# Kernel optimization log

Hardware: AMD Instinct MI355X
Metric: run time of the kernel (lower is better)

Reference implementation:

```python
import jax, jax.numpy as jnp
import numpy as np

D = 256; H = 4; HD = 64; WBAND = 64; KLOC = 8; EMAK = 256
SUMDECAY = 0.9; STATEDECAY = 0.9; STEP = 0.5


def _dwconv(x, kern, pad):
    # x: (B,T,D), kern: (D,1,K) cross-correlation taps, causal left pad
    lhs = jnp.transpose(x, (0, 2, 1))
    out = jax.lax.conv_general_dilated(
        lhs, kern, (1,), [(pad, 0)],
        dimension_numbers=('NCH', 'OIH', 'NCH'),
        feature_group_count=x.shape[-1])
    return jnp.transpose(out, (0, 2, 1))


def _ln(x, g, b):
    m = jnp.mean(x, -1, keepdims=True)
    v = jnp.var(x, -1, keepdims=True)
    return (x - m) * jax.lax.rsqrt(v + 1e-5) * g + b


def _lin(x, w, b):
    return jnp.dot(x, w.T) + b


def _forward(parallel_repr, sequential_state, trajectory_summary, conv_w, conv_b,
             qkv_w, qkv_b, mo_w, mo_b, fg_w, fg_b, gkv_w, gkv_b, go_w, go_b,
             comb_w, comb_b, ffn1_w, ffn1_b, ffn2_w, ffn2_b, tr1_w, tr1_b,
             tr2_w, tr2_b, p2s_w, p2s_b, s2p_w, s2p_b,
             ln1_g, ln1_b, ln2_g, ln2_b, ln3_g, ln3_b, ln4_g, ln4_b):
    B, T, _ = parallel_repr.shape
    # Tier 1: local depthwise causal conv (window 8); torch pads both sides then slices [:T] == causal left pad
    local_history = _dwconv(parallel_repr, conv_w, KLOC - 1) + conv_b
    # Tier 2: banded causal attention (keep j in [i-63, i])
    qkv = _lin(parallel_repr, qkv_w, qkv_b).reshape(B, T, 3, H, HD)
    qkv = jnp.transpose(qkv, (2, 0, 3, 1, 4))  # (3,B,H,T,HD)
    q, k, v = qkv[0], qkv[1], qkv[2]
    idx = jnp.arange(T)
    band = (idx[:, None] >= idx[None, :]) & (idx[None, :] > idx[:, None] - WBAND)
    scores = jnp.einsum('bhqd,bhkd->bhqk', q, k) / jnp.sqrt(jnp.float32(HD))
    attn = jax.nn.softmax(jnp.where(band, scores, -1e9), -1)
    med = jnp.einsum('bhqk,bhkd->bhqd', attn, v)
    med = jnp.transpose(med, (0, 2, 1, 3)).reshape(B, T, D)
    med = _lin(med, mo_w, mo_b)
    fg = jax.nn.sigmoid(_lin(jnp.concatenate([parallel_repr, med], -1), fg_w, fg_b))
    medium_out = med * fg
    # Tier 3: causal cumulative (linear-attention style) global concepts
    gkv = _lin(parallel_repr, gkv_w, gkv_b)
    gk, gv = jnp.split(gkv, 2, -1)
    gk = jax.nn.elu(gk) + 1.0
    concepts = jnp.cumsum(gk * gv, 1) / (jnp.cumsum(gk, 1) + 1e-5)
    global_out = _lin(concepts, go_w, go_b)
    combined = _lin(jnp.concatenate([local_history, medium_out, global_out], -1), comb_w, comb_b)
    pr = _ln(parallel_repr + combined, ln1_g, ln1_b)
    # EMA summary via 256-tap causal depthwise conv: w[i] = (1-d)*d^i
    kE = min(T, EMAK)
    taps = (1.0 - SUMDECAY) * SUMDECAY ** jnp.arange(kE, dtype=jnp.float32)
    kern = jnp.broadcast_to(taps[::-1][None, None, :], (D, 1, kE))
    global_summary = _dwconv(pr, kern, kE - 1)
    guidance = _lin(pr, p2s_w, p2s_b)
    cs = jnp.concatenate([pr + 0.3 * guidance, global_summary], -1)
    deltas = jnp.tanh(_lin(jax.nn.gelu(_lin(cs, tr1_w, tr1_b), approximate=False), tr2_w, tr2_b))
    scaled = deltas * STEP
    # state accumulation via conv trick: acc[t] = sum_i d^i * delta[t-i]
    staps = STATEDECAY ** jnp.arange(kE, dtype=jnp.float32)
    skern = jnp.broadcast_to(staps[::-1][None, None, :], (D, 1, kE))
    acc = _dwconv(scaled, skern, kE - 1)
    dpow = STATEDECAY ** jnp.arange(1, T + 1, dtype=jnp.float32)
    pre_ln = sequential_state[:, None, :] * dpow[None, :, None] + acc
    states = _ln(pre_ln, ln3_g, ln3_b)
    seq_g = _lin(states, s2p_w, s2p_b)
    ffn = _lin(jax.nn.gelu(_lin(pr + 0.3 * seq_g, ffn1_w, ffn1_b), approximate=False), ffn2_w, ffn2_b)
    pr_out = _ln(pr + ffn, ln2_g, ln2_b)
    final_state = _ln(states[:, -1, :], ln4_g, ln4_b)
    final_traj = global_summary[:, -1, :]
    return pr_out, final_state, final_traj


def setup_inputs():
    key = jax.random.key(0)
    ks = jax.random.split(key, 20)
    B, T = 4, 2048
    s = 0.02
    def w(i, shape):
        return jax.random.normal(ks[i], shape, jnp.float32) * s
    return {
        'parallel_repr': jax.random.normal(ks[0], (B, T, D), jnp.float32),
        'sequential_state': jax.random.normal(ks[1], (B, D), jnp.float32),
        'trajectory_summary': jax.random.normal(ks[2], (B, D), jnp.float32),
        'conv_w': w(3, (D, 1, KLOC)), 'conv_b': jnp.zeros((D,)),
        'qkv_w': w(4, (3 * D, D)), 'qkv_b': jnp.zeros((3 * D,)),
        'mo_w': w(5, (D, D)), 'mo_b': jnp.zeros((D,)),
        'fg_w': w(6, (D, 2 * D)), 'fg_b': jnp.zeros((D,)),
        'gkv_w': w(7, (2 * D, D)), 'gkv_b': jnp.zeros((2 * D,)),
        'go_w': w(8, (D, D)), 'go_b': jnp.zeros((D,)),
        'comb_w': w(9, (D, 3 * D)), 'comb_b': jnp.zeros((D,)),
        'ffn1_w': w(10, (4 * D, D)), 'ffn1_b': jnp.zeros((4 * D,)),
        'ffn2_w': w(11, (D, 4 * D)), 'ffn2_b': jnp.zeros((D,)),
        'tr1_w': w(12, (2 * D, 2 * D)), 'tr1_b': jnp.zeros((2 * D,)),
        'tr2_w': w(13, (D, 2 * D)), 'tr2_b': jnp.zeros((D,)),
        'p2s_w': w(14, (D, D)), 'p2s_b': jnp.zeros((D,)),
        's2p_w': w(15, (D, D)), 's2p_b': jnp.zeros((D,)),
        'ln1_g': jnp.ones((D,)), 'ln1_b': jnp.zeros((D,)),
        'ln2_g': jnp.ones((D,)), 'ln2_b': jnp.zeros((D,)),
        'ln3_g': jnp.ones((D,)), 'ln3_b': jnp.zeros((D,)),
        'ln4_g': jnp.ones((D,)), 'ln4_b': jnp.zeros((D,)),
    }


def reference(parallel_repr, sequential_state, trajectory_summary, conv_w, conv_b,
              qkv_w, qkv_b, mo_w, mo_b, fg_w, fg_b, gkv_w, gkv_b, go_w, go_b,
              comb_w, comb_b, ffn1_w, ffn1_b, ffn2_w, ffn2_b, tr1_w, tr1_b,
              tr2_w, tr2_b, p2s_w, p2s_b, s2p_w, s2p_b,
              ln1_g, ln1_b, ln2_g, ln2_b, ln3_g, ln3_b, ln4_g, ln4_b):
    return _forward(parallel_repr, sequential_state, trajectory_summary, conv_w, conv_b,
                    qkv_w, qkv_b, mo_w, mo_b, fg_w, fg_b, gkv_w, gkv_b, go_w, go_b,
                    comb_w, comb_b, ffn1_w, ffn1_b, ffn2_w, ffn2_b, tr1_w, tr1_b,
                    tr2_w, tr2_b, p2s_w, p2s_b, s2p_w, s2p_b,
                    ln1_g, ln1_b, ln2_g, ln2_b, ln3_g, ln3_b, ln4_g, ln4_b)
```

## Files before the change

kernel.cpp:

```cpp
#include <hip/hip_runtime.h>
#include <hip/hip_bf16.h>
#include <math.h>

#define D_  256
#define T_  2048
#define B_  4
#define M_  (B_*T_)
#define H_  4
#define HD_ 64

#define NC_ 64
#define LCH (T_/NC_)

enum { OP_NONE=0, OP_SIGMUL=1, OP_ADDAUX=2, OP_AXPBY=3, OP_GELU=4, OP_TANHHALF=5 };

typedef unsigned short u16;
typedef short short8 __attribute__((ext_vector_type(8)));
typedef float f32x4  __attribute__((ext_vector_type(4)));

__device__ __forceinline__ float gelu_f(float x){ return 0.5f*x*(1.0f+erff(x*0.70710678118654752f)); }
__device__ __forceinline__ float sigmoid_f(float x){ return 1.0f/(1.0f+expf(-x)); }

__device__ __forceinline__ unsigned pk2(float a, float b){
    __hip_bfloat162 h = __float22bfloat162_rn(make_float2(a,b));
    union { __hip_bfloat162 h; unsigned u; } c; c.h = h; return c.u;
}
__device__ __forceinline__ float bfu(u16 u){ return __uint_as_float(((unsigned)u)<<16); }
__device__ __forceinline__ u16 bf1(float x){ return (u16)(pk2(x,x)&0xffffu); }

#define OFF_QKV   0u
#define OFF_MO    327680u
#define OFF_FG    393216u
#define OFF_GO    524288u
#define OFF_COMB  589824u
#define OFF_FFN1  786432u
#define OFF_FFN2  1048576u
#define OFF_TR1   1310720u
#define OFF_TR2   1572864u
#define OFF_P2S   1703936u
#define OFF_S2P   1769472u
#define NWELEM    1835008u
#define NXELEM    2097152u
#define CVT_BLKS  3842u
#define CONV_BLKS 2048u

__global__ __launch_bounds__(256) void cvt_conv_k(
    const float* __restrict__ qkv_w, const float* __restrict__ gkv_w,
    const float* __restrict__ qkv_b, const float* __restrict__ gkv_b,
    const float* __restrict__ mo_w,  const float* __restrict__ fg_w,
    const float* __restrict__ go_w,  const float* __restrict__ comb_w,
    const float* __restrict__ ffn1_w,const float* __restrict__ ffn2_w,
    const float* __restrict__ tr1_w, const float* __restrict__ tr2_w,
    const float* __restrict__ p2s_w, const float* __restrict__ s2p_w,
    const float* __restrict__ X,
    const float* __restrict__ conv_w, const float* __restrict__ conv_b,
    u16* __restrict__ Wh, u16* __restrict__ Xh, float* __restrict__ bq,
    u16* __restrict__ LH)
{
    if (blockIdx.x >= CVT_BLKS){
        int idx = (blockIdx.x - CVT_BLKS)*256 + threadIdx.x;
        int d4 = (idx & 63) * 4;
        int bt = idx >> 6;
        int t = bt & (T_-1);
        float a0 = conv_b[d4], a1 = conv_b[d4+1], a2 = conv_b[d4+2], a3 = conv_b[d4+3];
        const float* xp = X + (size_t)bt*D_ + d4;
        #pragma unroll
        for (int j=0;j<8;++j){
            int tt = t - 7 + j;
            if (tt >= 0){
                float4 v = *(const float4*)(xp + (size_t)(j-7)*D_);
                a0 += v.x * conv_w[(d4+0)*8 + j];
                a1 += v.y * conv_w[(d4+1)*8 + j];
                a2 += v.z * conv_w[(d4+2)*8 + j];
                a3 += v.w * conv_w[(d4+3)*8 + j];
            }
        }
        *(uint2*)(LH + (size_t)bt*D_ + d4) = (uint2){ pk2(a0,a1), pk2(a2,a3) };
        return;
    }
    size_t i = ((size_t)blockIdx.x*256 + threadIdx.x)*4;
    if (i < NWELEM){
        const float* s; size_t base;
        if      (i < OFF_MO)  { s=(i<196608)?qkv_w:gkv_w; base=(i<196608)?0:196608; }
        else if (i < OFF_FG)  { s=mo_w;   base=OFF_MO; }
        else if (i < OFF_GO)  { s=fg_w;   base=OFF_FG; }
        else if (i < OFF_COMB){ s=go_w;   base=OFF_GO; }
        else if (i < OFF_FFN1){ s=comb_w; base=OFF_COMB; }
        else if (i < OFF_FFN2){ s=ffn1_w; base=OFF_FFN1; }
        else if (i < OFF_TR1) { s=ffn2_w; base=OFF_FFN2; }
        else if (i < OFF_TR2) { s=tr1_w;  base=OFF_TR1; }
        else if (i < OFF_P2S) { s=tr2_w;  base=OFF_TR2; }
        else if (i < OFF_S2P) { s=p2s_w;  base=OFF_P2S; }
        else                  { s=s2p_w;  base=OFF_S2P; }
        float4 v = *(const float4*)(s + (i-base));
        *(uint2*)(Wh + i) = (uint2){ pk2(v.x,v.y), pk2(v.z,v.w) };
    } else if (i < NWELEM + NXELEM){
        size_t j = i - NWELEM;
        float4 v = *(const float4*)(X + j);
        *(uint2*)(Xh + j) = (uint2){ pk2(v.x,v.y), pk2(v.z,v.w) };
    } else if (i < NWELEM + NXELEM + 1280){
        size_t j = i - (NWELEM + NXELEM);
        #pragma unroll
        for (int k=0;k<4;++k){
            size_t e = j + k;
            bq[e] = (e < 768) ? qkv_b[e] : gkv_b[e-768];
        }
    }
}

__global__ __launch_bounds__(512) void gemm_k(
    const u16* __restrict__ A0, const u16* __restrict__ W0, int ldw0, int K0,
    const u16* __restrict__ A1, const u16* __restrict__ W1, int ldw1, int K1,
    const u16* __restrict__ A2, const u16* __restrict__ W2, int ldw2, int K2,
    const float* __restrict__ bias, const void* __restrict__ aux, int aux_bf16,
    void* __restrict__ C, int ldc, int c_bf16, int op, int ncol)
{
    __shared__ u16 As[128*64];
    __shared__ u16 Ws[64*64];

    const int q8   = gridDim.x >> 3;
    const int lid  = (blockIdx.x & 7)*q8 + (blockIdx.x >> 3);
    const int brow = lid / ncol;
    const int bcol = lid - brow*ncol;
    const int row0 = brow*128, col0 = bcol*64;

    const int tid  = threadIdx.x;
    const int lane = tid & 63, wid = tid >> 6;
    const int wm = (wid >> 1)*32, wn = (wid & 1)*32;
    const int l15 = lane & 15, l4 = lane >> 4;
    const int rowA = tid >> 2;
    const int scA  = (tid & 3) * 8;
    const int rowW = tid >> 3;
    const int scW  = (tid & 7) * 8;

    f32x4 acc[2][2];
    #pragma unroll
    for (int i=0;i<2;++i)
        #pragma unroll
        for (int j=0;j<2;++j) acc[i][j] = (f32x4){0.f,0.f,0.f,0.f};

    uint4 ra0, ra1, rw0;

    auto loadtile = [&](const u16* A, const u16* W, int ldw, int K, int kb){
        const u16* ga = A + (size_t)(row0+rowA)*K + kb + scA;
        ra0 = *(const uint4*)ga;
        ra1 = *(const uint4*)(ga + 32);
        rw0 = *(const uint4*)(W + (size_t)(col0+rowW)*ldw + kb + scW);
    };
    auto storetile = [&](){
        const int sw = (rowA&7)<<3;
        *(uint4*)&As[(rowA*64 + scA) ^ sw]      = ra0;
        *(uint4*)&As[(rowA*64 + scA + 32) ^ sw] = ra1;
        *(uint4*)&Ws[(rowW*64 + scW) ^ ((rowW&7)<<3)] = rw0;
    };
    auto mfma_tile = [&](){
        #pragma unroll
        for (int ks=0;ks<2;++ks){
            const int koff = ks*32 + l4*8;
            short8 af[2], bf[2];
            #pragma unroll
            for (int f=0;f<2;++f){
                const int ar = wm + f*16 + l15;
                af[f] = *(const short8*)&As[(ar*64 + koff) ^ ((ar&7)<<3)];
                const int brn = wn + f*16 + l15;
                bf[f] = *(const short8*)&Ws[(brn*64 + koff) ^ ((brn&7)<<3)];
            }
            #pragma unroll
            for (int fm=0;fm<2;++fm)
                #pragma unroll
                for (int fn=0;fn<2;++fn)
                    acc[fm][fn] = __builtin_amdgcn_mfma_f32_16x16x32_bf16(
                        af[fm], bf[fn], acc[fm][fn], 0, 0, 0);
        }
    };

    const u16* Ac = A0; const u16* Wc = W0; int ldwc = ldw0, Kc = K0, kb = 0;
    loadtile(Ac, Wc, ldwc, Kc, 0);
    while (true){
        __syncthreads();
        storetile();
        __syncthreads();
        int nkb = kb + 64;
        const u16* nA = Ac; const u16* nW = Wc; int nld = ldwc, nK = Kc;
        bool have_next = true;
        if (nkb >= Kc){
            if (Ac == A0 && A1){ nA = A1; nW = W1; nld = ldw1; nK = K1; nkb = 0; }
            else if (Ac == A1 && A2){ nA = A2; nW = W2; nld = ldw2; nK = K2; nkb = 0; }
            else have_next = false;
        }
        if (have_next) loadtile(nA, nW, nld, nK, nkb);
        mfma_tile();
        if (!have_next) break;
        Ac = nA; Wc = nW; ldwc = nld; Kc = nK; kb = nkb;
    }

    #pragma unroll
    for (int fn=0;fn<2;++fn){
        const int n = col0 + wn + fn*16 + l15;
        const float bv = bias[n];
        #pragma unroll
        for (int fm=0;fm<2;++fm){
            #pragma unroll
            for (int j=0;j<4;++j){
                const int m = row0 + wm + fm*16 + l4*4 + j;
                float v = acc[fm][fn][j] + bv;
                if (op==OP_GELU)          v = gelu_f(v);
                else if (op==OP_TANHHALF) v = 0.5f*tanhf(v);
                else if (op!=OP_NONE){
                    const size_t ai = (size_t)m*D_ + n;
                    const float a = aux_bf16 ? bfu(((const u16*)aux)[ai])
                                             : ((const float*)aux)[ai];
                    if (op==OP_SIGMUL)      v = a*sigmoid_f(v);
                    else if (op==OP_ADDAUX) v = v + a;
                    else                    v = a + 0.3f*v;
                }
                if (c_bf16) ((u16*)C)[(size_t)m*ldc + n] = bf1(v);
                else        ((float*)C)[(size_t)m*ldc + n] = v;
            }
        }
    }
}

__global__ __launch_bounds__(256) void attn_k(const u16* __restrict__ QKVG,
    u16* __restrict__ MED)
{
    __shared__ u16 Kl[128*64];
    __shared__ u16 Ql[64*64];
    __shared__ u16 Vl[64*128];
    const int b = blockIdx.z, h = blockIdx.y;
    const int t0 = blockIdx.x * 64;
    const int kb0 = t0 - 64;
    const int tid = threadIdx.x;

    {
        const int r0 = tid >> 3, c8 = (tid & 7) * 8;
        #pragma unroll
        for (int rep=0;rep<4;++rep){
            const int r = r0 + rep*32;
            const int kg = kb0 + r;
            uint4 pk = {0,0,0,0}, pv = {0,0,0,0};
            if (kg >= 0){
                const u16* gp = QKVG + ((size_t)(b*T_ + kg))*1280 + h*HD_ + c8;
                pk = *(const uint4*)(gp + 256);
                pv = *(const uint4*)(gp + 512);
            }
            *(uint4*)&Kl[(r*64 + c8) ^ ((r&7)<<3)] = pk;
            const u16* pvu = (const u16*)&pv;
            #pragma unroll
            for (int j=0;j<8;++j){
                const int d = c8 + j;
                Vl[(d*128 + r) ^ ((d&15)<<3)] = pvu[j];
            }
        }
        #pragma unroll
        for (int rep=0;rep<2;++rep){
            const int r = r0 + rep*32;
            uint4 pq = *(const uint4*)(QKVG + ((size_t)(b*T_ + t0 + r))*1280 + h*HD_ + c8);
            *(uint4*)&Ql[(r*64 + c8) ^ ((r&7)<<3)] = pq;
        }
    }
    __syncthreads();

    const int lane = tid & 63, w = tid >> 6;
    const int l15 = lane & 15, l4 = lane >> 4;

    short8 bq[2];
    {
        const int qr = w*16 + l15;
        bq[0] = *(const short8*)&Ql[(qr*64 +      l4*8) ^ ((qr&7)<<3)];
        bq[1] = *(const short8*)&Ql[(qr*64 + 32 + l4*8) ^ ((qr&7)<<3)];
    }

    f32x4 s[8];
    #pragma unroll
    for (int kf=0;kf<8;++kf){
        const int kr = kf*16 + l15;
        short8 a0 = *(const short8*)&Kl[(kr*64 +      l4*8) ^ ((kr&7)<<3)];
        short8 a1 = *(const short8*)&Kl[(kr*64 + 32 + l4*8) ^ ((kr&7)<<3)];
        f32x4 acc = (f32x4){0.f,0.f,0.f,0.f};
        acc = __builtin_amdgcn_mfma_f32_16x16x32_bf16(a0, bq[0], acc, 0,0,0);
        acc = __builtin_amdgcn_mfma_f32_16x16x32_bf16(a1, bq[1], acc, 0,0,0);
        s[kf] = acc;
    }

    const int qg = t0 + w*16 + l15;
    float m = -1e30f;
    #pragma unroll
    for (int kf=0;kf<8;++kf){
        #pragma unroll
        for (int j=0;j<4;++j){
            const int kg = kb0 + kf*16 + l4*4 + j;
            const int diff = qg - kg;
            const float v = (kg >= 0 && diff >= 0 && diff < 64) ? s[kf][j]*0.125f : -1e30f;
            s[kf][j] = v;
            m = fmaxf(m, v);
        }
    }
    m = fmaxf(m, __shfl_xor(m,16));
    m = fmaxf(m, __shfl_xor(m,32));
    float lsum = 0.f;
    unsigned lo[8], hi[8];
    #pragma unroll
    for (int kf=0;kf<8;++kf){
        const float p0 = expf(s[kf][0]-m), p1 = expf(s[kf][1]-m);
        const float p2 = expf(s[kf][2]-m), p3 = expf(s[kf][3]-m);
        lsum += (p0+p1)+(p2+p3);
        lo[kf] = pk2(p0,p1);
        hi[kf] = pk2(p2,p3);
    }
    lsum += __shfl_xor(lsum,16);
    lsum += __shfl_xor(lsum,32);
    const float inv = 1.f/lsum;

    f32x4 o[4];
    #pragma unroll
    for (int df=0;df<4;++df) o[df] = (f32x4){0.f,0.f,0.f,0.f};
    const int baseLane = l15 + ((l4&1)<<5);
    const bool hiHalf = (l4>>1) != 0;
    #pragma unroll
    for (int kb=0;kb<4;++kb){
        const int x0 = __shfl((int)lo[2*kb],   baseLane);
        const int x1 = __shfl((int)hi[2*kb],   baseLane);
        const int x2 = __shfl((int)lo[2*kb],   baseLane+16);
        const int x3 = __shfl((int)hi[2*kb],   baseLane+16);
        const int y0 = __shfl((int)lo[2*kb+1], baseLane);
        const int y1 = __shfl((int)hi[2*kb+1], baseLane);
        const int y2 = __shfl((int)lo[2*kb+1], baseLane+16);
        const int y3 = __shfl((int)hi[2*kb+1], baseLane+16);
        int4 afi;
        afi.x = hiHalf ? y0 : x0;
        afi.y = hiHalf ? y1 : x1;
        afi.z = hiHalf ? y2 : x2;
        afi.w = hiHalf ? y3 : x3;
        union { int4 i; short8 s; } cv; cv.i = afi;
        #pragma unroll
        for (int df=0;df<4;++df){
            const int vr = df*16 + l15;
            short8 bv = *(const short8*)&Vl[(vr*128 + kb*32 + l4*8) ^ ((vr&15)<<3)];
            o[df] = __builtin_amdgcn_mfma_f32_16x16x32_bf16(cv.s, bv, o[df], 0,0,0);
        }
    }

    #pragma unroll
    for (int j=0;j<4;++j){
        const float invj = __shfl(inv, l4*4 + j);
        const int mrow = b*T_ + t0 + w*16 + l4*4 + j;
        u16* op = MED + (size_t)mrow*D_ + h*HD_ + l15;
        #pragma unroll
        for (int df=0;df<4;++df)
            op[df*16] = bf1(o[df][j] * invj);
    }
}

__global__ __launch_bounds__(256) void scan1_p1(const u16* __restrict__ QKVG,
    float* __restrict__ CA, float* __restrict__ CC)
{
    const int d = threadIdx.x, c = blockIdx.x, b = blockIdx.y;
    const u16* base = QKVG + ((size_t)(b*T_ + c*LCH))*1280;
    float sgk=0.f, sgkv=0.f;
    for (int t=0;t<LCH;++t){
        float gk = bfu(base[(size_t)t*1280 + 768 + d]);
        gk = gk > 0.f ? gk + 1.f : expf(gk);
        float gv = bfu(base[(size_t)t*1280 + 1024 + d]);
        sgk += gk; sgkv += gk*gv;
    }
    CA[((size_t)b*NC_ + c)*D_ + d] = sgk;
    CC[((size_t)b*NC_ + c)*D_ + d] = sgkv;
}

__global__ __launch_bounds__(256) void scan1_p3(const u16* __restrict__ QKVG,
    const float* __restrict__ CA, const float* __restrict__ CC, u16* __restrict__ CONC)
{
    const int d = threadIdx.x, c = blockIdx.x, b = blockIdx.y;
    float sgk = 0.f, sgkv = 0.f;
    for (int cc=0; cc<c; ++cc){
        sgk  += CA[((size_t)b*NC_ + cc)*D_ + d];
        sgkv += CC[((size_t)b*NC_ + cc)*D_ + d];
    }
    const u16* base = QKVG + ((size_t)(b*T_ + c*LCH))*1280;
    u16* out = CONC + ((size_t)(b*T_ + c*LCH))*D_ + d;
    for (int t=0;t<LCH;++t){
        float gk = bfu(base[(size_t)t*1280 + 768 + d]);
        gk = gk > 0.f ? gk + 1.f : expf(gk);
        float gv = bfu(base[(size_t)t*1280 + 1024 + d]);
        sgk += gk; sgkv += gk*gv;
        out[(size_t)t*D_] = bf1(sgkv / (sgk + 1e-5f));
    }
}

__global__ __launch_bounds__(256) void ema_p1h(const u16* __restrict__ X,
    float* __restrict__ CARRY, float alpha)
{
    const int d = threadIdx.x, c = blockIdx.x, b = blockIdx.y;
    const u16* xp = X + ((size_t)(b*T_ + c*LCH))*D_ + d;
    float g = 0.f;
    for (int t=0;t<LCH;++t) g = 0.9f*g + alpha*bfu(xp[(size_t)t*D_]);
    CARRY[((size_t)b*NC_ + c)*D_ + d] = g;
}

__global__ __launch_bounds__(256) void ema_p3h(const u16* __restrict__ X,
    const float* __restrict__ CARRY, u16* __restrict__ OUT, float alpha,
    float* __restrict__ traj)
{
    const int d = threadIdx.x, c = blockIdx.x, b = blockIdx.y;
    const float dL = powf(0.9f, (float)LCH);
    float g = 0.f;
    for (int cc=0; cc<c; ++cc) g = CARRY[((size_t)b*NC_ + cc)*D_ + d] + dL*g;
    const u16* xp = X + ((size_t)(b*T_ + c*LCH))*D_ + d;
    u16* op = OUT + ((size_t)(b*T_ + c*LCH))*D_ + d;
    for (int t=0;t<LCH;++t){
        g = 0.9f*g + alpha*bfu(xp[(size_t)t*D_]);
        op[(size_t)t*D_] = bf1(g);
    }
    if (c == NC_-1) traj[b*D_ + d] = g;
}

__global__ __launch_bounds__(256) void ln1ema_k(const u16* __restrict__ in,
    const float* __restrict__ g, const float* __restrict__ b,
    u16* __restrict__ out, float* __restrict__ CARRY)
{
    __shared__ float wacc[4][256];
    const int c = blockIdx.x, bb = blockIdx.y;
    const int w = threadIdx.x >> 6, lane = threadIdx.x & 63;
    const int db = lane*4;
    const int row0 = bb*T_ + c*LCH;
    float acc0=0.f, acc1=0.f, acc2=0.f, acc3=0.f;
    #pragma unroll
    for (int it=0; it<8; ++it){
        const int r = it*4 + w;
        uint2 u = *(const uint2*)(in + (size_t)(row0 + r)*D_ + db);
        float x0=bfu((u16)(u.x&0xffff)), x1=bfu((u16)(u.x>>16));
        float x2=bfu((u16)(u.y&0xffff)), x3=bfu((u16)(u.y>>16));
        float s  = x0+x1+x2+x3;
        float s2 = x0*x0+x1*x1+x2*x2+x3*x3;
        #pragma unroll
        for (int o=1;o<64;o<<=1){ s += __shfl_xor(s,o); s2 += __shfl_xor(s2,o); }
        float mean = s*(1.f/256.f);
        float var  = s2*(1.f/256.f) - mean*mean;
        float rs = rsqrtf(var + 1e-5f);
        float y0=(x0-mean)*rs*g[db+0]+b[db+0];
        float y1=(x1-mean)*rs*g[db+1]+b[db+1];
        float y2=(x2-mean)*rs*g[db+2]+b[db+2];
        float y3=(x3-mean)*rs*g[db+3]+b[db+3];
        *(uint2*)(out + (size_t)(row0+r)*D_ + db) = (uint2){ pk2(y0,y1), pk2(y2,y3) };
        const float wt = 0.1f*powf(0.9f, (float)(31-r));
        acc0 += wt*y0; acc1 += wt*y1; acc2 += wt*y2; acc3 += wt*y3;
    }
    wacc[w][db+0]=acc0; wacc[w][db+1]=acc1; wacc[w][db+2]=acc2; wacc[w][db+3]=acc3;
    __syncthreads();
    const int d = threadIdx.x;
    CARRY[((size_t)bb*NC_ + c)*D_ + d] =
        wacc[0][d] + wacc[1][d] + wacc[2][d] + wacc[3][d];
}

__global__ __launch_bounds__(256) void ema_ln3_k(const u16* __restrict__ X,
    const float* __restrict__ CARRY, const float* __restrict__ SEQ,
    const float* __restrict__ g3, const float* __restrict__ b3, u16* __restrict__ states,
    const float* __restrict__ g4, const float* __restrict__ b4, float* __restrict__ fsout)
{
    __shared__ float vals[LCH][256];
    __shared__ float mv[LCH][2];
    __shared__ float st4[256];
    __shared__ float red[8];
    const int d = threadIdx.x, c = blockIdx.x, bb = blockIdx.y;
    const float dL = powf(0.9f, (float)LCH);
    float a = 0.f;
    for (int cc=0; cc<c; ++cc) a = CARRY[((size_t)bb*NC_ + cc)*D_ + d] + dL*a;
    const float ss = SEQ[bb*D_ + d];
    float dp = powf(0.9f, (float)(c*LCH + 1));
    const u16* xp = X + ((size_t)(bb*T_ + c*LCH))*D_ + d;
    for (int t=0;t<LCH;++t){
        a = 0.9f*a + bfu(xp[(size_t)t*D_]);
        vals[t][d] = fmaf(ss, dp, a);
        dp *= 0.9f;
    }
    __syncthreads();
    {
        const int r = threadIdx.x >> 3, seg = threadIdx.x & 7;
        float s=0.f, s2=0.f;
        #pragma unroll
        for (int j=0;j<32;++j){ float v = vals[r][seg*32+j]; s += v; s2 += v*v; }
        s += __shfl_xor(s,1); s2 += __shfl_xor(s2,1);
        s += __shfl_xor(s,2); s2 += __shfl_xor(s2,2);
        s += __shfl_xor(s,4); s2 += __shfl_xor(s2,4);
        if (seg == 0){
            float mean = s*(1.f/256.f);
            float var  = s2*(1.f/256.f) - mean*mean;
            mv[r][0] = mean; mv[r][1] = rsqrtf(var + 1e-5f);
        }
    }
    __syncthreads();
    const float gd = g3[d], bd = b3[d];
    const bool isLast = (c == NC_-1);
    u16* sp = states + ((size_t)(bb*T_ + c*LCH))*D_ + d;
    for (int t=0;t<LCH;++t){
        float st = (vals[t][d] - mv[t][0])*mv[t][1]*gd + bd;
        sp[(size_t)t*D_] = bf1(st);
        if (isLast && t == LCH-1) st4[d] = st;
    }
    if (isLast){
        __syncthreads();
        float v = st4[d];
        float s = v, s2 = v*v;
        #pragma unroll
        for (int o=1;o<64;o<<=1){ s += __shfl_xor(s,o); s2 += __shfl_xor(s2,o); }
        if ((threadIdx.x & 63) == 0){ red[threadIdx.x>>6] = s; red[4+(threadIdx.x>>6)] = s2; }
        __syncthreads();
        float S  = red[0]+red[1]+red[2]+red[3];
        float S2 = red[4]+red[5]+red[6]+red[7];
        float m2 = S*(1.f/256.f);
        float r2 = rsqrtf(S2*(1.f/256.f) - m2*m2 + 1e-5f);
        fsout[bb*D_ + d] = (st4[d]-m2)*r2*g4[d] + b4[d];
    }
}

__global__ __launch_bounds__(256) void ln2h_k(const u16* __restrict__ in,
    const float* __restrict__ g, const float* __restrict__ b, float* __restrict__ out)
{
    int row  = blockIdx.x*4 + (threadIdx.x>>6);
    int lane = threadIdx.x & 63;
    uint2 u = *(const uint2*)(in + (size_t)row*D_ + lane*4);
    float x0=bfu((u16)(u.x&0xffff)), x1=bfu((u16)(u.x>>16));
    float x2=bfu((u16)(u.y&0xffff)), x3=bfu((u16)(u.y>>16));
    float s  = x0+x1+x2+x3;
    float s2 = x0*x0+x1*x1+x2*x2+x3*x3;
    #pragma unroll
    for (int o=1;o<64;o<<=1){ s += __shfl_xor(s,o); s2 += __shfl_xor(s2,o); }
    float mean = s * (1.f/256.f);
    float var  = s2 * (1.f/256.f) - mean*mean;
    float rs = rsqrtf(var + 1e-5f);
    int db = lane*4;
    float4 r;
    r.x=(x0-mean)*rs*g[db+0]+b[db+0];
    r.y=(x1-mean)*rs*g[db+1]+b[db+1];
    r.z=(x2-mean)*rs*g[db+2]+b[db+2];
    r.w=(x3-mean)*rs*g[db+3]+b[db+3];
    *(float4*)(out + (size_t)row*D_ + db) = r;
}

extern "C" void kernel_launch(void* const* d_in, const int* in_sizes, int n_in,
                              void* d_out, int out_size, void* d_ws, size_t ws_size,
                              hipStream_t stream)
{
    const float* X     = (const float*)d_in[0];
    const float* SEQ   = (const float*)d_in[1];
    const float* conv_w= (const float*)d_in[3];
    const float* conv_b= (const float*)d_in[4];
    const float* qkv_w = (const float*)d_in[5];
    const float* qkv_b = (const float*)d_in[6];
    const float* mo_w  = (const float*)d_in[7];
    const float* mo_b  = (const float*)d_in[8];
    const float* fg_w  = (const float*)d_in[9];
    const float* fg_b  = (const float*)d_in[10];
    const float* gkv_w = (const float*)d_in[11];
    const float* gkv_b = (const float*)d_in[12];
    const float* go_w  = (const float*)d_in[13];
    const float* go_b  = (const float*)d_in[14];
    const float* comb_w= (const float*)d_in[15];
    const float* comb_b= (const float*)d_in[16];
    const float* ffn1_w= (const float*)d_in[17];
    const float* ffn1_b= (const float*)d_in[18];
    const float* ffn2_w= (const float*)d_in[19];
    const float* ffn2_b= (const float*)d_in[20];
    const float* tr1_w = (const float*)d_in[21];
    const float* tr1_b = (const float*)d_in[22];
    const float* tr2_w = (const float*)d_in[23];
    const float* tr2_b = (const float*)d_in[24];
    const float* p2s_w = (const float*)d_in[25];
    const float* p2s_b = (const float*)d_in[26];
    const float* s2p_w = (const float*)d_in[27];
    const float* s2p_b = (const float*)d_in[28];
    const float* ln1_g = (const float*)d_in[29];
    const float* ln1_b = (const float*)d_in[30];
    const float* ln2_g = (const float*)d_in[31];
    const float* ln2_b = (const float*)d_in[32];
    const float* ln3_g = (const float*)d_in[33];
    const float* ln3_b = (const float*)d_in[34];
    const float* ln4_g = (const float*)d_in[35];
    const float* ln4_b = (const float*)d_in[36];

    char* p = (char*)d_ws;
    auto alloc = [&](size_t bytes)->char*{ char* r = p; p += (bytes + 255) & ~(size_t)255; return r; };

    u16*   QKVG = (u16*)  alloc((size_t)M_*1280*2);
    u16*   Wh   = (u16*)  alloc((size_t)NWELEM*2);
    float* bq   = (float*)alloc(1280*4);
    u16*   Xh   = (u16*)  alloc((size_t)M_*256*2);
    u16*   MED  = (u16*)  alloc((size_t)M_*256*2);
    u16*   MED2 = (u16*)  alloc((size_t)M_*256*2);
    u16*   LH   = (u16*)  alloc((size_t)M_*256*2);
    u16*   CONC = (u16*)  alloc((size_t)M_*256*2);
    u16*   GOUT = (u16*)  alloc((size_t)M_*256*2);
    u16*   MOUT = (u16*)  alloc((size_t)M_*256*2);
    u16*   PRE1h= (u16*)  alloc((size_t)M_*256*2);
    u16*   PRh  = (u16*)  alloc((size_t)M_*256*2);
    u16*   GSUM = (u16*)  alloc((size_t)M_*256*2);
    u16*   CS1  = (u16*)  alloc((size_t)M_*256*2);
    u16*   H1   = (u16*)  alloc((size_t)M_*512*2);
    u16*   SCALEDh=(u16*) alloc((size_t)M_*256*2);
    u16*   STATESh=(u16*) alloc((size_t)M_*256*2);
    u16*   FFNIN= (u16*)  alloc((size_t)M_*256*2);
    u16*   H2   = (u16*)  alloc((size_t)M_*1024*2);
    u16*   PRE2h= (u16*)  alloc((size_t)M_*256*2);
    float* CAR0 = (float*)alloc((size_t)B_*NC_*D_*4);
    float* CAR1 = (float*)alloc((size_t)B_*NC_*D_*4);

    float* out_pr = (float*)d_out;
    float* out_fs = out_pr + (size_t)M_*256;
    float* out_tj = out_fs + B_*256;

    const dim3 blk256(256), blk512(512);
    const dim3 scan_grid(NC_, B_);
    const int NRg = M_/128;

    cvt_conv_k<<<dim3(CVT_BLKS + CONV_BLKS), blk256, 0, stream>>>(
        qkv_w, gkv_w, qkv_b, gkv_b, mo_w, fg_w, go_w, comb_w,
        ffn1_w, ffn2_w, tr1_w, tr2_w, p2s_w, s2p_w, X, conv_w, conv_b,
        Wh, Xh, bq, LH);
    gemm_k<<<dim3(NRg*20), blk512, 0, stream>>>(
        Xh, Wh+OFF_QKV, 256, 256,  nullptr,nullptr,0,0,  nullptr,nullptr,0,0,
        bq, nullptr, 0, QKVG, 1280, 1, OP_NONE, 20);
    attn_k<<<dim3(T_/64, H_, B_), blk256, 0, stream>>>(QKVG, MED);
    gemm_k<<<dim3(NRg*4), blk512, 0, stream>>>(
        MED, Wh+OFF_MO, 256, 256,  nullptr,nullptr,0,0,  nullptr,nullptr,0,0,
        mo_b, nullptr, 0, MED2, 256, 1, OP_NONE, 4);
    scan1_p1<<<scan_grid, blk256, 0, stream>>>(QKVG, CAR0, CAR1);
    scan1_p3<<<scan_grid, blk256, 0, stream>>>(QKVG, CAR0, CAR1, CONC);
    gemm_k<<<dim3(NRg*4), blk512, 0, stream>>>(
        CONC, Wh+OFF_GO, 256, 256,  nullptr,nullptr,0,0,  nullptr,nullptr,0,0,
        go_b, nullptr, 0, GOUT, 256, 1, OP_NONE, 4);
    gemm_k<<<dim3(NRg*4), blk512, 0, stream>>>(
        Xh, Wh+OFF_FG, 512, 256,  MED2, Wh+OFF_FG+256, 512, 256,  nullptr,nullptr,0,0,
        fg_b, MED2, 1, MOUT, 256, 1, OP_SIGMUL, 4);
    gemm_k<<<dim3(NRg*4), blk512, 0, stream>>>(
        LH, Wh+OFF_COMB, 768, 256,  MOUT, Wh+OFF_COMB+256, 768, 256,  GOUT, Wh+OFF_COMB+512, 768, 256,
        comb_b, X, 0, PRE1h, 256, 1, OP_ADDAUX, 4);
    ln1ema_k<<<scan_grid, blk256, 0, stream>>>(PRE1h, ln1_g, ln1_b, PRh, CAR0);
    ema_p3h<<<scan_grid, blk256, 0, stream>>>(PRh, CAR0, GSUM, 0.1f, out_tj);
    gemm_k<<<dim3(NRg*4), blk512, 0, stream>>>(
        PRh, Wh+OFF_P2S, 256, 256,  nullptr,nullptr,0,0,  nullptr,nullptr,0,0,
        p2s_b, PRh, 1, CS1, 256, 1, OP_AXPBY, 4);
    gemm_k<<<dim3(NRg*8), blk512, 0, stream>>>(
        CS1, Wh+OFF_TR1, 512, 256,  GSUM, Wh+OFF_TR1+256, 512, 256,  nullptr,nullptr,0,0,
        tr1_b, nullptr, 0, H1, 512, 1, OP_GELU, 8);
    gemm_k<<<dim3(NRg*4), blk512, 0, stream>>>(
        H1, Wh+OFF_TR2, 512, 512,  nullptr,nullptr,0,0,  nullptr,nullptr,0,0,
        tr2_b, nullptr, 0, SCALEDh, 256, 1, OP_TANHHALF, 4);
    ema_p1h<<<scan_grid, blk256, 0, stream>>>(SCALEDh, CAR0, 1.0f);
    ema_ln3_k<<<scan_grid, blk256, 0, stream>>>(
        SCALEDh, CAR0, SEQ, ln3_g, ln3_b, STATESh, ln4_g, ln4_b, out_fs);
    gemm_k<<<dim3(NRg*4), blk512, 0, stream>>>(
        STATESh, Wh+OFF_S2P, 256, 256,  nullptr,nullptr,0,0,  nullptr,nullptr,0,0,
        s2p_b, PRh, 1, FFNIN, 256, 1, OP_AXPBY, 4);
    gemm_k<<<dim3(NRg*16), blk512, 0, stream>>>(
        FFNIN, Wh+OFF_FFN1, 256, 256,  nullptr,nullptr,0,0,  nullptr,nullptr,0,0,
        ffn1_b, nullptr, 0, H2, 1024, 1, OP_GELU, 16);
    gemm_k<<<dim3(NRg*4), blk512, 0, stream>>>(
        H2, Wh+OFF_FFN2, 1024, 1024,  nullptr,nullptr,0,0,  nullptr,nullptr,0,0,
        ffn2_b, PRh, 1, PRE2h, 256, 1, OP_ADDAUX, 4);
    ln2h_k<<<dim3(M_/4), blk256, 0, stream>>>(PRE2h, ln2_g, ln2_b, out_pr);
}
```

Before: 253.4 us.

## Co-schedule scan and EMA phases as extra blocks inside attention and GEMM launches

Folds the scan pass-1 into the attention kernel as extra blocks, the scan pass-3 into the MO-projection GEMM launch, and the EMA pass-3 into the P2S GEMM launch, using a block-index split. This removes three separate launches and lets the latency-bound serial scans run alongside independent GEMM/attention blocks. The cost is extra kernel arguments and branching in the GEMM. The fused tail blocks use only 256 of 512 threads, and they may extend the tail of each launch if they are scheduled last.

```diff
diff --git a/kernel.cpp b/kernel.cpp
--- a/kernel.cpp
+++ b/kernel.cpp
@@ -113,12 +113,51 @@
     const u16* __restrict__ A1, const u16* __restrict__ W1, int ldw1, int K1,
     const u16* __restrict__ A2, const u16* __restrict__ W2, int ldw2, int K2,
     const float* __restrict__ bias, const void* __restrict__ aux, int aux_bf16,
-    void* __restrict__ C, int ldc, int c_bf16, int op, int ncol)
-{
+    void* __restrict__ C, int ldc, int c_bf16, int op, int ncol,
+    int gemmBlocks, int tailOp,
+    const u16* __restrict__ tIn, const float* __restrict__ tC0,
+    const float* __restrict__ tC1, u16* __restrict__ tOut, float* __restrict__ tTraj)
+{
+    if ((int)blockIdx.x >= gemmBlocks){
+        if (threadIdx.x < 256){
+            const int j = blockIdx.x - gemmBlocks;
+            const int c = j & (NC_-1), b = j >> 6;
+            const int d = threadIdx.x;
+            if (tailOp == 1){
+                float sgk = 0.f, sgkv = 0.f;
+                for (int cc=0; cc<c; ++cc){
+                    sgk  += tC0[((size_t)b*NC_ + cc)*D_ + d];
+                    sgkv += tC1[((size_t)b*NC_ + cc)*D_ + d];
+                }
+                const u16* base = tIn + ((size_t)(b*T_ + c*LCH))*1280;
+                u16* out = tOut + ((size_t)(b*T_ + c*LCH))*D_ + d;
+                for (int t=0;t<LCH;++t){
+                    float gk = bfu(base[(size_t)t*1280 + 768 + d]);
+                    gk = gk > 0.f ? gk + 1.f : expf(gk);
+                    float gv = bfu(base[(size_t)t*1280 + 1024 + d]);
+                    sgk += gk; sgkv += gk*gv;
+                    out[(size_t)t*D_] = bf1(sgkv / (sgk + 1e-5f));
+                }
+            } else {
+                const float dL = powf(0.9f, (float)LCH);
+                float g = 0.f;
+                for (int cc=0; cc<c; ++cc) g = tC0[((size_t)b*NC_ + cc)*D_ + d] + dL*g;
+                const u16* xp = tIn + ((size_t)(b*T_ + c*LCH))*D_ + d;
+                u16* op2 = tOut + ((size_t)(b*T_ + c*LCH))*D_ + d;
+                for (int t=0;t<LCH;++t){
+                    g = 0.9f*g + 0.1f*bfu(xp[(size_t)t*D_]);
+                    op2[(size_t)t*D_] = bf1(g);
+                }
+                if (c == NC_-1) tTraj[b*D_ + d] = g;
+            }
+        }
+        return;
+    }
+
     __shared__ u16 As[128*64];
     __shared__ u16 Ws[64*64];
 
-    const int q8   = gridDim.x >> 3;
+    const int q8   = gemmBlocks >> 3;
     const int lid  = (blockIdx.x & 7)*q8 + (blockIdx.x >> 3);
     const int brow = lid / ncol;
     const int bcol = lid - brow*ncol;
@@ -221,16 +260,33 @@
     }
 }
 
-__global__ __launch_bounds__(256) void attn_k(const u16* __restrict__ QKVG,
-    u16* __restrict__ MED)
-{
+__global__ __launch_bounds__(256) void attn_scan_k(const u16* __restrict__ QKVG,
+    u16* __restrict__ MED, float* __restrict__ CA, float* __restrict__ CC)
+{
+    const int tid = threadIdx.x;
+    if (blockIdx.x >= 512){
+        const int j = blockIdx.x - 512;
+        const int c = j & (NC_-1), b = j >> 6;
+        const int d = tid;
+        const u16* base = QKVG + ((size_t)(b*T_ + c*LCH))*1280;
+        float sgk=0.f, sgkv=0.f;
+        for (int t=0;t<LCH;++t){
+            float gk = bfu(base[(size_t)t*1280 + 768 + d]);
+            gk = gk > 0.f ? gk + 1.f : expf(gk);
+            float gv = bfu(base[(size_t)t*1280 + 1024 + d]);
+            sgk += gk; sgkv += gk*gv;
+        }
+        CA[((size_t)b*NC_ + c)*D_ + d] = sgk;
+        CC[((size_t)b*NC_ + c)*D_ + d] = sgkv;
+        return;
+    }
+
     __shared__ u16 Kl[128*64];
     __shared__ u16 Ql[64*64];
     __shared__ u16 Vl[64*128];
-    const int b = blockIdx.z, h = blockIdx.y;
-    const int t0 = blockIdx.x * 64;
+    const int b = blockIdx.x >> 7, h = (blockIdx.x >> 5) & 3;
+    const int t0 = (blockIdx.x & 31) * 64;
     const int kb0 = t0 - 64;
-    const int tid = threadIdx.x;
 
     {
         const int r0 = tid >> 3, c8 = (tid & 7) * 8;
@@ -352,42 +408,6 @@
     }
 }
 
-__global__ __launch_bounds__(256) void scan1_p1(const u16* __restrict__ QKVG,
-    float* __restrict__ CA, float* __restrict__ CC)
-{
-    const int d = threadIdx.x, c = blockIdx.x, b = blockIdx.y;
-    const u16* base = QKVG + ((size_t)(b*T_ + c*LCH))*1280;
-    float sgk=0.f, sgkv=0.f;
-    for (int t=0;t<LCH;++t){
-        float gk = bfu(base[(size_t)t*1280 + 768 + d]);
-        gk = gk > 0.f ? gk + 1.f : expf(gk);
-        float gv = bfu(base[(size_t)t*1280 + 1024 + d]);
-        sgk += gk; sgkv += gk*gv;
-    }
-    CA[((size_t)b*NC_ + c)*D_ + d] = sgk;
-    CC[((size_t)b*NC_ + c)*D_ + d] = sgkv;
-}
-
-__global__ __launch_bounds__(256) void scan1_p3(const u16* __restrict__ QKVG,
-    const float* __restrict__ CA, const float* __restrict__ CC, u16* __restrict__ CONC)
-{
-    const int d = threadIdx.x, c = blockIdx.x, b = blockIdx.y;
-    float sgk = 0.f, sgkv = 0.f;
-    for (int cc=0; cc<c; ++cc){
-        sgk  += CA[((size_t)b*NC_ + cc)*D_ + d];
-        sgkv += CC[((size_t)b*NC_ + cc)*D_ + d];
-    }
-    const u16* base = QKVG + ((size_t)(b*T_ + c*LCH))*1280;
-    u16* out = CONC + ((size_t)(b*T_ + c*LCH))*D_ + d;
-    for (int t=0;t<LCH;++t){
-        float gk = bfu(base[(size_t)t*1280 + 768 + d]);
-        gk = gk > 0.f ? gk + 1.f : expf(gk);
-        float gv = bfu(base[(size_t)t*1280 + 1024 + d]);
-        sgk += gk; sgkv += gk*gv;
-        out[(size_t)t*D_] = bf1(sgkv / (sgk + 1e-5f));
-    }
-}
-
 __global__ __launch_bounds__(256) void ema_p1h(const u16* __restrict__ X,
     float* __restrict__ CARRY, float alpha)
 {
@@ -396,23 +416,6 @@
     float g = 0.f;
     for (int t=0;t<LCH;++t) g = 0.9f*g + alpha*bfu(xp[(size_t)t*D_]);
     CARRY[((size_t)b*NC_ + c)*D_ + d] = g;
-}
-
-__global__ __launch_bounds__(256) void ema_p3h(const u16* __restrict__ X,
-    const float* __restrict__ CARRY, u16* __restrict__ OUT, float alpha,
-    float* __restrict__ traj)
-{
-    const int d = threadIdx.x, c = blockIdx.x, b = blockIdx.y;
-    const float dL = powf(0.9f, (float)LCH);
-    float g = 0.f;
-    for (int cc=0; cc<c; ++cc) g = CARRY[((size_t)b*NC_ + cc)*D_ + d] + dL*g;
-    const u16* xp = X + ((size_t)(b*T_ + c*LCH))*D_ + d;
-    u16* op = OUT + ((size_t)(b*T_ + c*LCH))*D_ + d;
-    for (int t=0;t<LCH;++t){
-        g = 0.9f*g + alpha*bfu(xp[(size_t)t*D_]);
-        op[(size_t)t*D_] = bf1(g);
-    }
-    if (c == NC_-1) traj[b*D_ + d] = g;
 }
 
 __global__ __launch_bounds__(256) void ln1ema_k(const u16* __restrict__ in,
@@ -619,44 +622,52 @@
         Wh, Xh, bq, LH);
     gemm_k<<<dim3(NRg*20), blk512, 0, stream>>>(
         Xh, Wh+OFF_QKV, 256, 256,  nullptr,nullptr,0,0,  nullptr,nullptr,0,0,
-        bq, nullptr, 0, QKVG, 1280, 1, OP_NONE, 20);
-    attn_k<<<dim3(T_/64, H_, B_), blk256, 0, stream>>>(QKVG, MED);
-    gemm_k<<<dim3(NRg*4), blk512, 0, stream>>>(
+        bq, nullptr, 0, QKVG, 1280, 1, OP_NONE, 20,
+        NRg*20, 0, nullptr, nullptr, nullptr, nullptr, nullptr);
+    attn_scan_k<<<dim3(512 + 256), blk256, 0, stream>>>(QKVG, MED, CAR0, CAR1);
+    gemm_k<<<dim3(NRg*4 + 256), blk512, 0, stream>>>(
         MED, Wh+OFF_MO, 256, 256,  nullptr,nullptr,0,0,  nullptr,nullptr,0,0,
-        mo_b, nullptr, 0, MED2, 256, 1, OP_NONE, 4);
-    scan1_p1<<<scan_grid, blk256, 0, stream>>>(QKVG, CAR0, CAR1);
-    scan1_p3<<<scan_grid, blk256, 0, stream>>>(QKVG, CAR0, CAR1, CONC);
+        mo_b, nullptr, 0, MED2, 256, 1, OP_NONE, 4,
+        NRg*4, 1, QKVG, CAR0, CAR1, CONC, nullptr);
     gemm_k<<<dim3(NRg*4), blk512, 0, stream>>>(
         CONC, Wh+OFF_GO, 256, 256,  nullptr,nullptr,0,0,  nullptr,nullptr,0,0,
-        go_b, nullptr, 0, GOUT, 256, 1, OP_NONE, 4);
+        go_b, nullptr, 0, GOUT, 256, 1, OP_NONE, 4,
+        NRg*4, 0, nullptr, nullptr, nullptr, nullptr, nullptr);
     gemm_k<<<dim3(NRg*4), blk512, 0, stream>>>(
         Xh, Wh+OFF_FG, 512, 256,  MED2, Wh+OFF_FG+256, 512, 256,  nullptr,nullptr,0,0,
-        fg_b, MED2, 1, MOUT, 256, 1, OP_SIGMUL, 4);
+        fg_b, MED2, 1, MOUT, 256, 1, OP_SIGMUL, 4,
+        NRg*4, 0, nullptr, nullptr, nullptr, nullptr, nullptr);
     gemm_k<<<dim3(NRg*4), blk512, 0, stream>>>(
         LH, Wh+OFF_COMB, 768, 256,  MOUT, Wh+OFF_COMB+256, 768, 256,  GOUT, Wh+OFF_COMB+512, 768, 256,
-        comb_b, X, 0, PRE1h, 256, 1, OP_ADDAUX, 4);
+        comb_b, X, 0, PRE1h, 256, 1, OP_ADDAUX, 4,
+        NRg*4, 0, nullptr, nullptr, nullptr, nullptr, nullptr);
     ln1ema_k<<<scan_grid, blk256, 0, stream>>>(PRE1h, ln1_g, ln1_b, PRh, CAR0);
-    ema_p3h<<<scan_grid, blk256, 0, stream>>>(PRh, CAR0, GSUM, 0.1f, out_tj);
-    gemm_k<<<dim3(NRg*4), blk512, 0, stream>>>(
+    gemm_k<<<dim3(NRg*4 + 256), blk512, 0, stream>>>(
         PRh, Wh+OFF_P2S, 256, 256,  nullptr,nullptr,0,0,  nullptr,nullptr,0,0,
-        p2s_b, PRh, 1, CS1, 256, 1, OP_AXPBY, 4);
+        p2s_b, PRh, 1, CS1, 256, 1, OP_AXPBY, 4,
+        NRg*4, 2, PRh, CAR0, nullptr, GSUM, out_tj);
     gemm_k<<<dim3(NRg*8), blk512, 0, stream>>>(
         CS1, Wh+OFF_TR1, 512, 256,  GSUM, Wh+OFF_TR1+256, 512, 256,  nullptr,nullptr,0,0,
-        tr1_b, nullptr, 0, H1, 512, 1, OP_GELU, 8);
+        tr1_b, nullptr, 0, H1, 512, 1, OP_GELU, 8,
+        NRg*8, 0, nullptr, nullptr, nullptr, nullptr, nullptr);
     gemm_k<<<dim3(NRg*4), blk512, 0, stream>>>(
         H1, Wh+OFF_TR2, 512, 512,  nullptr,nullptr,0,0,  nullptr,nullptr,0,0,
-        tr2_b, nullptr, 0, SCALEDh, 256, 1, OP_TANHHALF, 4);
+        tr2_b, nullptr, 0, SCALEDh, 256, 1, OP_TANHHALF, 4,
+        NRg*4, 0, nullptr, nullptr, nullptr, nullptr, nullptr);
     ema_p1h<<<scan_grid, blk256, 0, stream>>>(SCALEDh, CAR0, 1.0f);
     ema_ln3_k<<<scan_grid, blk256, 0, stream>>>(
         SCALEDh, CAR0, SEQ, ln3_g, ln3_b, STATESh, ln4_g, ln4_b, out_fs);
     gemm_k<<<dim3(NRg*4), blk512, 0, stream>>>(
         STATESh, Wh+OFF_S2P, 256, 256,  nullptr,nullptr,0,0,  nullptr,nullptr,0,0,
-        s2p_b, PRh, 1, FFNIN, 256, 1, OP_AXPBY, 4);
+        s2p_b, PRh, 1, FFNIN, 256, 1, OP_AXPBY, 4,
+        NRg*4, 0, nullptr, nullptr, nullptr, nullptr, nullptr);
     gemm_k<<<dim3(NRg*16), blk512, 0, stream>>>(
         FFNIN, Wh+OFF_FFN1, 256, 256,  nullptr,nullptr,0,0,  nullptr,nullptr,0,0,
-        ffn1_b, nullptr, 0, H2, 1024, 1, OP_GELU, 16);
+        ffn1_b, nullptr, 0, H2, 1024, 1, OP_GELU, 16,
+        NRg*16, 0, nullptr, nullptr, nullptr, nullptr, nullptr);
     gemm_k<<<dim3(NRg*4), blk512, 0, stream>>>(
         H2, Wh+OFF_FFN2, 1024, 1024,  nullptr,nullptr,0,0,  nullptr,nullptr,0,0,
-        ffn2_b, PRh, 1, PRE2h, 256, 1, OP_ADDAUX, 4);
+        ffn2_b, PRh, 1, PRE2h, 256, 1, OP_ADDAUX, 4,
+        NRg*4, 0, nullptr, nullptr, nullptr, nullptr, nullptr);
     ln2h_k<<<dim3(M_/4), blk256, 0, stream>>>(PRE2h, ln2_g, ln2_b, out_pr);
 }
```

New measurement: 238.6 us. -5.8%, faster.
